# Optimization experiments

Measured on AMD Instinct MI355X. Metric: run time of the kernel, lower is better.

Reference implementation:

```python
import jax, jax.numpy as jnp
import numpy as np

N0, N1, N2 = 1200000, 120000, 12000  # nodes per hop (outermost -> seeds)
E0, E1 = 1200000, 120000
IN_C, HID_C, OUT_C = 256, 256, 64


def setup_inputs() -> dict:
    key = jax.random.key(0)
    ks = jax.random.split(key, 10)
    s_in, s_hid = 1.0 / np.sqrt(IN_C), 1.0 / np.sqrt(HID_C)
    return {
        "x": jax.random.normal(ks[0], (N0, IN_C), dtype=jnp.float32),
        "src0": jax.random.randint(ks[1], (E0,), 0, N0, dtype=jnp.int64),
        "dst0": jax.random.randint(ks[2], (E0,), 0, N1, dtype=jnp.int64),
        "src1": jax.random.randint(ks[3], (E1,), 0, N1, dtype=jnp.int64),
        "dst1": jax.random.randint(ks[4], (E1,), 0, N2, dtype=jnp.int64),
        "Wl0": jax.random.normal(ks[5], (HID_C, IN_C), dtype=jnp.float32) * s_in,
        "b0": jnp.zeros((HID_C,), dtype=jnp.float32),
        "Wr0": jax.random.normal(ks[6], (HID_C, IN_C), dtype=jnp.float32) * s_in,
        "Wl1": jax.random.normal(ks[7], (OUT_C, HID_C), dtype=jnp.float32) * s_hid,
        "b1": jnp.zeros((OUT_C,), dtype=jnp.float32),
        "Wr1": jax.random.normal(ks[8], (OUT_C, HID_C), dtype=jnp.float32) * s_hid,
    }


def _sage_conv(x_src, x_tgt, src, dst, Wl, b, Wr, n_tgt):
    # gather neighbor (source) features, mean-scatter onto targets
    msg = x_src[src]                                          # [E, C]
    agg = jax.ops.segment_sum(msg, dst, num_segments=n_tgt)   # [n_tgt, C]
    cnt = jax.ops.segment_sum(jnp.ones((dst.shape[0],), x_src.dtype), dst,
                              num_segments=n_tgt)
    agg = agg / jnp.maximum(cnt, 1.0)[:, None]
    return agg @ Wl.T + b + x_tgt @ Wr.T


def reference(x, src0, dst0, src1, dst1, Wl0, b0, Wr0, Wl1, b1, Wr1):
    # layer 0 (eval mode: dropout is identity)
    h = _sage_conv(x, x[:N1], src0, dst0, Wl0, b0, Wr0, N1)
    h = jax.nn.relu(h)
    # layer 1
    out = _sage_conv(h, h[:N2], src1, dst1, Wl1, b1, Wr1, N2)
    return jax.nn.log_softmax(out, axis=-1)
```

## Files before the change

### kernel.cpp

```cpp
#include <hip/hip_runtime.h>
#include <stdint.h>

#define N0c 1200000
#define N1c 120000
#define N2c 12000
#define E0c 1200000
#define E1c 120000
#define NB0 118
#define NB1 12
#define N1pad 120064
#define N2pad 12032
#define ROWB 80
#define ROWU 40

typedef short short8 __attribute__((ext_vector_type(8)));
typedef float f32x4 __attribute__((ext_vector_type(4)));
typedef unsigned short u16;

__device__ __forceinline__ u16 f2bf(float f) {
    union { float f; unsigned u; } v; v.f = f;
    unsigned r = v.u + 0x7FFFu + ((v.u >> 16) & 1u);
    return (u16)(r >> 16);
}
__device__ __forceinline__ float bf2f(u16 h) {
    union { unsigned u; float f; } v; v.u = ((unsigned)h) << 16;
    return v.f;
}

__device__ __forceinline__ void gload16(const char* g, char* l) {
    __builtin_amdgcn_global_load_lds(
        (const __attribute__((address_space(1))) void*)g,
        (__attribute__((address_space(3))) void*)l, 16, 0, 0);
}

__global__ void k_hist(const int* __restrict__ dst0, const int* __restrict__ dst1,
                       int* __restrict__ c0, int* __restrict__ c1) {
    int i = blockIdx.x * 256 + threadIdx.x;
    int part = blockIdx.x & 7;
    if (i < E0c) atomicAdd(&c0[part * N1c + dst0[i]], 1);
    else if (i < E0c + E1c) atomicAdd(&c1[part * N2c + dst1[i - E0c]], 1);
}

__global__ void k_scanA(const int* __restrict__ c0, const int* __restrict__ c1,
                        int* __restrict__ partials) {
    __shared__ int sh[256];
    int hop = blockIdx.x >= NB0;
    int blk = hop ? blockIdx.x - NB0 : blockIdx.x;
    const int* c = hop ? c1 : c0;
    int n = hop ? N2c : N1c;
    int d0 = blk * 1024 + threadIdx.x * 4;
    int tsum = 0;
#pragma unroll
    for (int j = 0; j < 4; ++j) {
        int d = d0 + j;
        if (d < n)
#pragma unroll
            for (int k = 0; k < 8; ++k) tsum += c[k * n + d];
    }
    sh[threadIdx.x] = tsum;
    __syncthreads();
    for (int ofs = 128; ofs > 0; ofs >>= 1) {
        if (threadIdx.x < ofs) sh[threadIdx.x] += sh[threadIdx.x + ofs];
        __syncthreads();
    }
    if (threadIdx.x == 0) partials[blockIdx.x] = sh[0];
}

__global__ void k_scanB(int* __restrict__ partials, int* __restrict__ rs0,
                        int* __restrict__ rs1) {
    __shared__ int sh[256];
    int tid = threadIdx.x;
    int v0 = tid < NB0 ? partials[tid] : 0;
    sh[tid] = v0; __syncthreads();
    for (int ofs = 1; ofs < 256; ofs <<= 1) {
        int t = tid >= ofs ? sh[tid - ofs] : 0;
        __syncthreads();
        sh[tid] += t;
        __syncthreads();
    }
    if (tid < NB0) partials[tid] = sh[tid] - v0;
    __syncthreads();
    int v1 = tid < NB1 ? partials[NB0 + tid] : 0;
    sh[tid] = v1; __syncthreads();
    for (int ofs = 1; ofs < 256; ofs <<= 1) {
        int t = tid >= ofs ? sh[tid - ofs] : 0;
        __syncthreads();
        sh[tid] += t;
        __syncthreads();
    }
    if (tid < NB1) partials[NB0 + tid] = sh[tid] - v1;
    if (tid == 0) { rs0[N1c] = E0c; rs1[N2c] = E1c; }
}

__global__ void k_scanC(const int* __restrict__ c0, const int* __restrict__ c1,
                        const int* __restrict__ partials, int* __restrict__ rs0,
                        int* __restrict__ rs1, int* __restrict__ bs0,
                        int* __restrict__ bs1) {
    __shared__ int sh[256];
    int hop = blockIdx.x >= NB0;
    int blk = hop ? blockIdx.x - NB0 : blockIdx.x;
    const int* c = hop ? c1 : c0;
    int* rs = hop ? rs1 : rs0;
    int* bs = hop ? bs1 : bs0;
    int n = hop ? N2c : N1c;
    int tid = threadIdx.x;
    int d0 = blk * 1024 + tid * 4;
    int cv[4][8];
    int tsum = 0;
#pragma unroll
    for (int j = 0; j < 4; ++j)
#pragma unroll
        for (int k = 0; k < 8; ++k) {
            int d = d0 + j;
            int v = (d < n) ? c[k * n + d] : 0;
            cv[j][k] = v; tsum += v;
        }
    sh[tid] = tsum; __syncthreads();
    for (int ofs = 1; ofs < 256; ofs <<= 1) {
        int t = tid >= ofs ? sh[tid - ofs] : 0;
        __syncthreads();
        sh[tid] += t;
        __syncthreads();
    }
    int run = partials[blockIdx.x] + sh[tid] - tsum;
#pragma unroll
    for (int j = 0; j < 4; ++j) {
        int d = d0 + j;
        if (d < n) {
            rs[d] = run;
#pragma unroll
            for (int k = 0; k < 8; ++k) { bs[k * n + d] = run; run += cv[j][k]; }
        }
    }
}

__global__ void k_scat(const int* __restrict__ src0, const int* __restrict__ dst0,
                       const int* __restrict__ src1, const int* __restrict__ dst1,
                       int* __restrict__ c0, int* __restrict__ c1,
                       const int* __restrict__ bs0, const int* __restrict__ bs1,
                       int* __restrict__ eidx0, int* __restrict__ eidx1) {
    int i = blockIdx.x * 256 + threadIdx.x;
    int part = blockIdx.x & 7;
    if (i < E0c) {
        int d = dst0[i];
        int off = atomicSub(&c0[part * N1c + d], 1) - 1;
        eidx0[bs0[part * N1c + d] + off] = src0[i];
    } else if (i < E0c + E1c) {
        int j = i - E0c;
        int d = dst1[j];
        int off = atomicSub(&c1[part * N2c + d], 1) - 1;
        eidx1[bs1[part * N2c + d] + off] = src1[j];
    }
}

__global__ void k_wcat2(u16* __restrict__ Bt0, const float* __restrict__ Wl0,
                        const float* __restrict__ Wr0, u16* __restrict__ Bt1,
                        const float* __restrict__ Wl1, const float* __restrict__ Wr1) {
    int i = blockIdx.x * blockDim.x + threadIdx.x;
    if (i < 256 * 512) {
        int c = i >> 9, k = i & 511;
        float v = (k < 256) ? Wl0[c * 256 + k] : Wr0[c * 256 + (k - 256)];
        Bt0[((size_t)(k >> 5) * 256 + c) * ROWU + (k & 31)] = f2bf(v);
    } else if (i < 256 * 512 + 128 * 512) {
        int j = i - 256 * 512;
        int c = j >> 9, k = j & 511;
        float v = 0.f;
        if (c < 64) v = (k < 256) ? Wl1[c * 256 + k] : Wr1[c * 256 + (k - 256)];
        Bt1[j] = f2bf(v);
    }
}

__global__ void k_agg0(const float* __restrict__ x, const int* __restrict__ eidx,
                       const int* __restrict__ rs, u16* __restrict__ A, int ntgt) {
    int w = (int)((blockIdx.x * blockDim.x + threadIdx.x) >> 6);
    int lane = threadIdx.x & 63;
    if (w >= ntgt) return;
    int s = rs[w], e = rs[w + 1];
    float a0 = 0.f, a1 = 0.f, a2 = 0.f, a3 = 0.f;
    int i = s;
    for (; i + 8 <= e; i += 8) {
        float4 v[8];
#pragma unroll
        for (int u = 0; u < 8; ++u)
            v[u] = ((const float4*)(x + (long)eidx[i + u] * 256))[lane];
#pragma unroll
        for (int u = 0; u < 8; ++u) {
            a0 += v[u].x; a1 += v[u].y; a2 += v[u].z; a3 += v[u].w;
        }
    }
    for (; i + 2 <= e; i += 2) {
        float4 v0 = ((const float4*)(x + (long)eidx[i] * 256))[lane];
        float4 v1 = ((const float4*)(x + (long)eidx[i + 1] * 256))[lane];
        a0 += v0.x + v1.x; a1 += v0.y + v1.y; a2 += v0.z + v1.z; a3 += v0.w + v1.w;
    }
    if (i < e) {
        float4 v = ((const float4*)(x + (long)eidx[i] * 256))[lane];
        a0 += v.x; a1 += v.y; a2 += v.z; a3 += v.w;
    }
    int c = e - s; if (c < 1) c = 1;
    float sc = 1.f / (float)c;
    int kt = lane >> 3;
    int cu = (lane & 7) * 4;
    ushort4 oa;
    oa.x = f2bf(a0 * sc); oa.y = f2bf(a1 * sc); oa.z = f2bf(a2 * sc); oa.w = f2bf(a3 * sc);
    *(ushort4*)(A + ((size_t)kt * N1pad + w) * ROWU + cu) = oa;
    float4 sv = ((const float4*)(x + (long)w * 256))[lane];
    ushort4 os;
    os.x = f2bf(sv.x); os.y = f2bf(sv.y); os.z = f2bf(sv.z); os.w = f2bf(sv.w);
    *(ushort4*)(A + ((size_t)(kt + 8) * N1pad + w) * ROWU + cu) = os;
}

__global__ void k_agg1(const u16* __restrict__ hsrc, const int* __restrict__ eidx,
                       const int* __restrict__ rs, u16* __restrict__ A, int ntgt) {
    int w = (int)((blockIdx.x * blockDim.x + threadIdx.x) >> 6);
    int lane = threadIdx.x & 63;
    if (w >= ntgt) return;
    int s = rs[w], e = rs[w + 1];
    float a0 = 0.f, a1 = 0.f, a2 = 0.f, a3 = 0.f;
    int i = s;
    for (; i + 4 <= e; i += 4) {
        ushort4 v0 = ((const ushort4*)(hsrc + (long)eidx[i] * 256))[lane];
        ushort4 v1 = ((const ushort4*)(hsrc + (long)eidx[i + 1] * 256))[lane];
        ushort4 v2 = ((const ushort4*)(hsrc + (long)eidx[i + 2] * 256))[lane];
        ushort4 v3 = ((const ushort4*)(hsrc + (long)eidx[i + 3] * 256))[lane];
        a0 += (bf2f(v0.x) + bf2f(v1.x)) + (bf2f(v2.x) + bf2f(v3.x));
        a1 += (bf2f(v0.y) + bf2f(v1.y)) + (bf2f(v2.y) + bf2f(v3.y));
        a2 += (bf2f(v0.z) + bf2f(v1.z)) + (bf2f(v2.z) + bf2f(v3.z));
        a3 += (bf2f(v0.w) + bf2f(v1.w)) + (bf2f(v2.w) + bf2f(v3.w));
    }
    for (; i < e; ++i) {
        ushort4 v = ((const ushort4*)(hsrc + (long)eidx[i] * 256))[lane];
        a0 += bf2f(v.x); a1 += bf2f(v.y); a2 += bf2f(v.z); a3 += bf2f(v.w);
    }
    int c = e - s; if (c < 1) c = 1;
    float sc = 1.f / (float)c;
    ushort4 o;
    o.x = f2bf(a0 * sc); o.y = f2bf(a1 * sc); o.z = f2bf(a2 * sc); o.w = f2bf(a3 * sc);
    *(ushort4*)(A + (long)w * 512 + lane * 4) = o;
    ushort4 sv = ((const ushort4*)(hsrc + (long)w * 256))[lane];
    *(ushort4*)(A + (long)w * 512 + 256 + lane * 4) = sv;
}

__global__ __launch_bounds__(512)
void k_gemm0(const u16* __restrict__ A0, const u16* __restrict__ Bt,
             const float* __restrict__ bias, u16* __restrict__ outp) {
    __shared__ int4 Lbuf[2 * 30720 / 16];
    char* L = (char*)Lbuf;
    const int tid = threadIdx.x;
    const int lane = tid & 63, wid = tid >> 6;
    const int wm = wid >> 2, wn = wid & 3;
    const long m0 = (long)blockIdx.x * 128;

    f32x4 acc[4][4];
#pragma unroll
    for (int i = 0; i < 4; ++i)
#pragma unroll
        for (int j = 0; j < 4; ++j) acc[i][j] = (f32x4){0.f, 0.f, 0.f, 0.f};

    const char* Abase = (const char*)A0 + m0 * ROWB;
    const char* Bbase = (const char*)Bt;

    auto stage = [&](int buf, int kt) {
        char* lb = L + buf * 30720;
        const char* ga = Abase + (size_t)kt * ((size_t)N1pad * ROWB);
        const char* gb = Bbase + (size_t)kt * (256 * ROWB);
#pragma unroll
        for (int c0 = 0; c0 < 4; ++c0) {
            int c = wid + c0 * 8;
            if (c < 30) {
                const char* g = (c < 10) ? (ga + c * 1024) : (gb + (c - 10) * 1024);
                gload16(g + lane * 16, lb + c * 1024);
            }
        }
    };

    stage(0, 0);
    const int rr = lane & 15, gg = lane >> 4;
    for (int ks = 0; ks < 16; ++ks) {
        int cur = ks & 1;
        __syncthreads();
        if (ks + 1 < 16) stage(cur ^ 1, ks + 1);
        const char* lb = L + cur * 30720;
        short8 af[4], bv[4];
#pragma unroll
        for (int f = 0; f < 4; ++f) {
            af[f] = *(const short8*)(lb + (wm * 64 + f * 16 + rr) * ROWB + gg * 16);
            bv[f] = *(const short8*)(lb + 10240 + (wn * 64 + f * 16 + rr) * ROWB + gg * 16);
        }
#pragma unroll
        for (int i = 0; i < 4; ++i)
#pragma unroll
            for (int j = 0; j < 4; ++j)
                acc[i][j] =
                    __builtin_amdgcn_mfma_f32_16x16x32_bf16(af[i], bv[j], acc[i][j], 0, 0, 0);
    }

#pragma unroll
    for (int j = 0; j < 4; ++j) {
        int col = wn * 64 + j * 16 + rr;
        float bvl = bias[col];
#pragma unroll
        for (int i = 0; i < 4; ++i) {
            long row = m0 + wm * 64 + i * 16 + gg * 4;
#pragma unroll
            for (int q = 0; q < 4; ++q) {
                long r = row + q;
                if (r < N1c) {
                    float v = acc[i][j][q] + bvl;
                    v = v > 0.f ? v : 0.f;
                    outp[r * 256 + col] = f2bf(v);
                }
            }
        }
    }
}

#define BM 128
#define BK 32
#define LDK 40

template <int WN, bool RELU_BF16>
__global__ __launch_bounds__(128 * WN)
void k_gemm(const u16* __restrict__ A, const u16* __restrict__ Bt,
            const float* __restrict__ bias, void* __restrict__ outp,
            int M, int Ncols, int ldo) {
    constexpr int BN_ = WN * 64;
    constexpr int APT = 4 / WN;
    constexpr int WSH = (WN == 4) ? 2 : 1;
    __shared__ u16 As[BM * LDK];
    __shared__ u16 Bs[BN_ * LDK];
    const int tid = threadIdx.x;
    const int lane = tid & 63, wid = tid >> 6;
    const int wm = wid >> WSH, wn = wid & (WN - 1);
    const long m0 = (long)blockIdx.x * BM;
    const int n0 = blockIdx.y * BN_;
    const int sar = tid / WN, sac = (tid % WN) * (APT * 8);
    const int sbr = tid >> 1, sbc = (tid & 1) * 16;

    f32x4 acc[4][4];
#pragma unroll
    for (int i = 0; i < 4; ++i)
#pragma unroll
        for (int j = 0; j < 4; ++j) acc[i][j] = (f32x4){0.f, 0.f, 0.f, 0.f};

    int4 ra[APT]; int4 rb[2];

    auto load_tile = [&](int ks) {
        int k0 = ks * BK;
        const int4* p = (const int4*)(A + (m0 + sar) * 512 + k0 + sac);
#pragma unroll
        for (int t = 0; t < APT; ++t) ra[t] = p[t];
        const int4* q = (const int4*)(Bt + (long)(n0 + sbr) * 512 + k0 + sbc);
        rb[0] = q[0]; rb[1] = q[1];
    };

    auto write_tile = [&]() {
        int4* da = (int4*)(As + sar * LDK + sac);
#pragma unroll
        for (int t = 0; t < APT; ++t) da[t] = ra[t];
        int4* db = (int4*)(Bs + sbr * LDK + sbc);
        db[0] = rb[0]; db[1] = rb[1];
    };

    load_tile(0);
    const int NK = 512 / BK;
    for (int ks = 0; ks < NK; ++ks) {
        __syncthreads();
        write_tile();
        __syncthreads();
        if (ks + 1 < NK) load_tile(ks + 1);
        short8 af[4], bv[4];
        const int rr = lane & 15, gg = lane >> 4;
#pragma unroll
        for (int f = 0; f < 4; ++f) {
            af[f] = *(const short8*)(As + (wm * 64 + f * 16 + rr) * LDK + gg * 8);
            bv[f] = *(const short8*)(Bs + (wn * 64 + f * 16 + rr) * LDK + gg * 8);
        }
#pragma unroll
        for (int i = 0; i < 4; ++i)
#pragma unroll
            for (int j = 0; j < 4; ++j)
                acc[i][j] =
                    __builtin_amdgcn_mfma_f32_16x16x32_bf16(af[i], bv[j], acc[i][j], 0, 0, 0);
    }

#pragma unroll
    for (int j = 0; j < 4; ++j) {
        int col = n0 + wn * 64 + j * 16 + (lane & 15);
        if (col >= Ncols) continue;
        float bvl = bias[col];
#pragma unroll
        for (int i = 0; i < 4; ++i) {
            long row = m0 + wm * 64 + i * 16 + (lane >> 4) * 4;
#pragma unroll
            for (int q = 0; q < 4; ++q) {
                long r = row + q;
                if (r < M) {
                    float v = acc[i][j][q] + bvl;
                    if (RELU_BF16) {
                        v = v > 0.f ? v : 0.f;
                        ((u16*)outp)[r * (long)ldo + col] = f2bf(v);
                    } else {
                        ((float*)outp)[r * (long)ldo + col] = v;
                    }
                }
            }
        }
    }
}

__global__ void k_lsm(const float* __restrict__ lg, float* __restrict__ out, int nrows) {
    int w = (int)((blockIdx.x * blockDim.x + threadIdx.x) >> 6);
    int lane = threadIdx.x & 63;
    if (w >= nrows) return;
    float v = lg[(long)w * 64 + lane];
    float m = v;
    for (int d = 32; d > 0; d >>= 1) m = fmaxf(m, __shfl_xor(m, d, 64));
    float ex = __expf(v - m);
    float s = ex;
    for (int d = 32; d > 0; d >>= 1) s += __shfl_xor(s, d, 64);
    out[(long)w * 64 + lane] = v - m - __logf(s);
}

extern "C" void kernel_launch(void* const* d_in, const int* in_sizes, int n_in,
                              void* d_out, int out_size, void* d_ws, size_t ws_size,
                              hipStream_t stream) {
    const float* x   = (const float*)d_in[0];
    const int* src0  = (const int*)d_in[1];
    const int* dst0  = (const int*)d_in[2];
    const int* src1  = (const int*)d_in[3];
    const int* dst1  = (const int*)d_in[4];
    const float* Wl0 = (const float*)d_in[5];
    const float* b0  = (const float*)d_in[6];
    const float* Wr0 = (const float*)d_in[7];
    const float* Wl1 = (const float*)d_in[8];
    const float* b1  = (const float*)d_in[9];
    const float* Wr1 = (const float*)d_in[10];

    char* base = (char*)d_ws;
    size_t off = 0;
    auto alloc = [&](size_t bytes) -> void* {
        off = (off + 255) & ~(size_t)255;
        void* p = base + off;
        off += bytes;
        return p;
    };
    int* c0       = (int*)alloc((size_t)8 * N1c * 4);
    int* c1       = (int*)alloc((size_t)8 * N2c * 4);
    int* bs0      = (int*)alloc((size_t)8 * N1c * 4);
    int* bs1      = (int*)alloc((size_t)8 * N2c * 4);
    int* rs0      = (int*)alloc((size_t)(N1c + 1) * 4);
    int* rs1      = (int*)alloc((size_t)(N2c + 1) * 4);
    int* partials = (int*)alloc((size_t)(NB0 + NB1) * 4);
    int* eidx0    = (int*)alloc((size_t)E0c * 4);
    int* eidx1    = (int*)alloc((size_t)E1c * 4);
    u16* A0       = (u16*)alloc((size_t)16 * N1pad * ROWU * 2);
    u16* hbuf     = (u16*)alloc((size_t)N1pad * 256 * 2);
    u16* A1       = (u16*)alloc((size_t)N2pad * 512 * 2);
    u16* Bt0      = (u16*)alloc((size_t)16 * 256 * ROWU * 2);
    u16* Bt1      = (u16*)alloc((size_t)128 * 512 * 2);
    float* logits = (float*)alloc((size_t)N2pad * 64 * 4);

    hipMemsetAsync(c0, 0, (size_t)8 * (N1c + N2c) * 4, stream);

    const int Etot = E0c + E1c;
    k_hist<<<(Etot + 255) / 256, 256, 0, stream>>>(dst0, dst1, c0, c1);
    k_scanA<<<NB0 + NB1, 256, 0, stream>>>(c0, c1, partials);
    k_scanB<<<1, 256, 0, stream>>>(partials, rs0, rs1);
    k_scanC<<<NB0 + NB1, 256, 0, stream>>>(c0, c1, partials, rs0, rs1, bs0, bs1);
    k_scat<<<(Etot + 255) / 256, 256, 0, stream>>>(src0, dst0, src1, dst1,
                                                   c0, c1, bs0, bs1, eidx0, eidx1);

    k_wcat2<<<(256 * 512 + 128 * 512 + 255) / 256, 256, 0, stream>>>(Bt0, Wl0, Wr0,
                                                                     Bt1, Wl1, Wr1);

    k_agg0<<<(N1c + 3) / 4, 256, 0, stream>>>(x, eidx0, rs0, A0, N1c);
    k_gemm0<<<N1pad / 128, 512, 0, stream>>>(A0, Bt0, b0, hbuf);

    k_agg1<<<(N2c + 3) / 4, 256, 0, stream>>>(hbuf, eidx1, rs1, A1, N2c);
    dim3 g1(N2pad / BM, 1);
    k_gemm<2, false><<<g1, 256, 0, stream>>>(A1, Bt1, b1, logits, N2c, 64, 64);

    k_lsm<<<(N2c + 3) / 4, 256, 0, stream>>>(logits, (float*)d_out, N2c);
}
```

Measured before the change: 584.7 us.

## Fuse weight prep into histogram, self-features into GEMM0, log-softmax into GEMM1

Merges the weight conversion kernel into the histogram launch as extra blocks. The layer-0 self-feature bf16 conversion moves from the aggregation kernel into the GEMM0 staging path, which now reads x directly for the upper K tiles. This halves the A0 buffer and removes a write and re-read. It also specializes the second GEMM with a fused bias and log-softmax epilogue, dropping the logits buffer and the separate softmax kernel. Gather loads in agg0 switch to nontemporal loads, which risks worse cache behaviour for repeated source rows, and GEMM0 staging now does synchronous register loads for half its K tiles.

```diff
diff --git a/kernel.cpp b/kernel.cpp
--- a/kernel.cpp
+++ b/kernel.cpp
@@ -12,6 +12,8 @@
 #define N2pad 12032
 #define ROWB 80
 #define ROWU 40
+#define HB 5157
+#define WCB 768
 
 typedef short short8 __attribute__((ext_vector_type(8)));
 typedef float f32x4 __attribute__((ext_vector_type(4)));
@@ -22,10 +24,6 @@
     unsigned r = v.u + 0x7FFFu + ((v.u >> 16) & 1u);
     return (u16)(r >> 16);
 }
-__device__ __forceinline__ float bf2f(u16 h) {
-    union { unsigned u; float f; } v; v.u = ((unsigned)h) << 16;
-    return v.f;
-}
 
 __device__ __forceinline__ void gload16(const char* g, char* l) {
     __builtin_amdgcn_global_load_lds(
@@ -34,11 +32,29 @@
 }
 
 __global__ void k_hist(const int* __restrict__ dst0, const int* __restrict__ dst1,
-                       int* __restrict__ c0, int* __restrict__ c1) {
-    int i = blockIdx.x * 256 + threadIdx.x;
-    int part = blockIdx.x & 7;
-    if (i < E0c) atomicAdd(&c0[part * N1c + dst0[i]], 1);
-    else if (i < E0c + E1c) atomicAdd(&c1[part * N2c + dst1[i - E0c]], 1);
+                       int* __restrict__ c0, int* __restrict__ c1,
+                       u16* __restrict__ Bt0, const float* __restrict__ Wl0,
+                       const float* __restrict__ Wr0, u16* __restrict__ Bt1,
+                       const float* __restrict__ Wl1, const float* __restrict__ Wr1) {
+    if (blockIdx.x < HB) {
+        int i = blockIdx.x * 256 + threadIdx.x;
+        int part = blockIdx.x & 7;
+        if (i < E0c) atomicAdd(&c0[part * N1c + dst0[i]], 1);
+        else if (i < E0c + E1c) atomicAdd(&c1[part * N2c + dst1[i - E0c]], 1);
+    } else {
+        int i = (blockIdx.x - HB) * 256 + threadIdx.x;
+        if (i < 256 * 512) {
+            int c = i >> 9, k = i & 511;
+            float v = (k < 256) ? Wl0[c * 256 + k] : Wr0[c * 256 + (k - 256)];
+            Bt0[((size_t)(k >> 5) * 256 + c) * ROWU + (k & 31)] = f2bf(v);
+        } else {
+            int j = i - 256 * 512;
+            int c = j >> 9, k = j & 511;
+            float v = 0.f;
+            if (c < 64) v = (k < 256) ? Wl1[c * 256 + k] : Wr1[c * 256 + (k - 256)];
+            Bt1[j] = f2bf(v);
+        }
+    }
 }
 
 __global__ void k_scanA(const int* __restrict__ c0, const int* __restrict__ c1,
@@ -153,23 +169,6 @@
     }
 }
 
-__global__ void k_wcat2(u16* __restrict__ Bt0, const float* __restrict__ Wl0,
-                        const float* __restrict__ Wr0, u16* __restrict__ Bt1,
-                        const float* __restrict__ Wl1, const float* __restrict__ Wr1) {
-    int i = blockIdx.x * blockDim.x + threadIdx.x;
-    if (i < 256 * 512) {
-        int c = i >> 9, k = i & 511;
-        float v = (k < 256) ? Wl0[c * 256 + k] : Wr0[c * 256 + (k - 256)];
-        Bt0[((size_t)(k >> 5) * 256 + c) * ROWU + (k & 31)] = f2bf(v);
-    } else if (i < 256 * 512 + 128 * 512) {
-        int j = i - 256 * 512;
-        int c = j >> 9, k = j & 511;
-        float v = 0.f;
-        if (c < 64) v = (k < 256) ? Wl1[c * 256 + k] : Wr1[c * 256 + (k - 256)];
-        Bt1[j] = f2bf(v);
-    }
-}
-
 __global__ void k_agg0(const float* __restrict__ x, const int* __restrict__ eidx,
                        const int* __restrict__ rs, u16* __restrict__ A, int ntgt) {
     int w = (int)((blockIdx.x * blockDim.x + threadIdx.x) >> 6);
@@ -179,23 +178,28 @@
     float a0 = 0.f, a1 = 0.f, a2 = 0.f, a3 = 0.f;
     int i = s;
     for (; i + 8 <= e; i += 8) {
-        float4 v[8];
+        f32x4 v[8];
 #pragma unroll
         for (int u = 0; u < 8; ++u)
-            v[u] = ((const float4*)(x + (long)eidx[i + u] * 256))[lane];
+            v[u] = __builtin_nontemporal_load(
+                ((const f32x4*)(x + (long)eidx[i + u] * 256)) + lane);
 #pragma unroll
         for (int u = 0; u < 8; ++u) {
-            a0 += v[u].x; a1 += v[u].y; a2 += v[u].z; a3 += v[u].w;
+            a0 += v[u][0]; a1 += v[u][1]; a2 += v[u][2]; a3 += v[u][3];
         }
     }
     for (; i + 2 <= e; i += 2) {
-        float4 v0 = ((const float4*)(x + (long)eidx[i] * 256))[lane];
-        float4 v1 = ((const float4*)(x + (long)eidx[i + 1] * 256))[lane];
-        a0 += v0.x + v1.x; a1 += v0.y + v1.y; a2 += v0.z + v1.z; a3 += v0.w + v1.w;
+        f32x4 v0 = __builtin_nontemporal_load(
+            ((const f32x4*)(x + (long)eidx[i] * 256)) + lane);
+        f32x4 v1 = __builtin_nontemporal_load(
+            ((const f32x4*)(x + (long)eidx[i + 1] * 256)) + lane);
+        a0 += v0[0] + v1[0]; a1 += v0[1] + v1[1];
+        a2 += v0[2] + v1[2]; a3 += v0[3] + v1[3];
     }
     if (i < e) {
-        float4 v = ((const float4*)(x + (long)eidx[i] * 256))[lane];
-        a0 += v.x; a1 += v.y; a2 += v.z; a3 += v.w;
+        f32x4 v = __builtin_nontemporal_load(
+            ((const f32x4*)(x + (long)eidx[i] * 256)) + lane);
+        a0 += v[0]; a1 += v[1]; a2 += v[2]; a3 += v[3];
     }
     int c = e - s; if (c < 1) c = 1;
     float sc = 1.f / (float)c;
@@ -204,10 +208,6 @@
     ushort4 oa;
     oa.x = f2bf(a0 * sc); oa.y = f2bf(a1 * sc); oa.z = f2bf(a2 * sc); oa.w = f2bf(a3 * sc);
     *(ushort4*)(A + ((size_t)kt * N1pad + w) * ROWU + cu) = oa;
-    float4 sv = ((const float4*)(x + (long)w * 256))[lane];
-    ushort4 os;
-    os.x = f2bf(sv.x); os.y = f2bf(sv.y); os.z = f2bf(sv.z); os.w = f2bf(sv.w);
-    *(ushort4*)(A + ((size_t)(kt + 8) * N1pad + w) * ROWU + cu) = os;
 }
 
 __global__ void k_agg1(const u16* __restrict__ hsrc, const int* __restrict__ eidx,
@@ -217,20 +217,23 @@
     if (w >= ntgt) return;
     int s = rs[w], e = rs[w + 1];
     float a0 = 0.f, a1 = 0.f, a2 = 0.f, a3 = 0.f;
+    auto acc4 = [&](ushort4 v) {
+        union { unsigned u; float f; } c0, c1, c2, c3;
+        c0.u = (unsigned)v.x << 16; c1.u = (unsigned)v.y << 16;
+        c2.u = (unsigned)v.z << 16; c3.u = (unsigned)v.w << 16;
+        a0 += c0.f; a1 += c1.f; a2 += c2.f; a3 += c3.f;
+    };
     int i = s;
     for (; i + 4 <= e; i += 4) {
         ushort4 v0 = ((const ushort4*)(hsrc + (long)eidx[i] * 256))[lane];
         ushort4 v1 = ((const ushort4*)(hsrc + (long)eidx[i + 1] * 256))[lane];
         ushort4 v2 = ((const ushort4*)(hsrc + (long)eidx[i + 2] * 256))[lane];
         ushort4 v3 = ((const ushort4*)(hsrc + (long)eidx[i + 3] * 256))[lane];
-        a0 += (bf2f(v0.x) + bf2f(v1.x)) + (bf2f(v2.x) + bf2f(v3.x));
-        a1 += (bf2f(v0.y) + bf2f(v1.y)) + (bf2f(v2.y) + bf2f(v3.y));
-        a2 += (bf2f(v0.z) + bf2f(v1.z)) + (bf2f(v2.z) + bf2f(v3.z));
-        a3 += (bf2f(v0.w) + bf2f(v1.w)) + (bf2f(v2.w) + bf2f(v3.w));
+        acc4(v0); acc4(v1); acc4(v2); acc4(v3);
     }
     for (; i < e; ++i) {
         ushort4 v = ((const ushort4*)(hsrc + (long)eidx[i] * 256))[lane];
-        a0 += bf2f(v.x); a1 += bf2f(v.y); a2 += bf2f(v.z); a3 += bf2f(v.w);
+        acc4(v);
     }
     int c = e - s; if (c < 1) c = 1;
     float sc = 1.f / (float)c;
@@ -242,8 +245,9 @@
 }
 
 __global__ __launch_bounds__(512)
-void k_gemm0(const u16* __restrict__ A0, const u16* __restrict__ Bt,
-             const float* __restrict__ bias, u16* __restrict__ outp) {
+void k_gemm0(const u16* __restrict__ A0, const float* __restrict__ x,
+             const u16* __restrict__ Bt, const float* __restrict__ bias,
+             u16* __restrict__ outp) {
     __shared__ int4 Lbuf[2 * 30720 / 16];
     char* L = (char*)Lbuf;
     const int tid = threadIdx.x;
@@ -259,18 +263,35 @@
 
     const char* Abase = (const char*)A0 + m0 * ROWB;
     const char* Bbase = (const char*)Bt;
+    const int srow = tid >> 2, scq = tid & 3;
 
     auto stage = [&](int buf, int kt) {
         char* lb = L + buf * 30720;
-        const char* ga = Abase + (size_t)kt * ((size_t)N1pad * ROWB);
         const char* gb = Bbase + (size_t)kt * (256 * ROWB);
-#pragma unroll
-        for (int c0 = 0; c0 < 4; ++c0) {
-            int c = wid + c0 * 8;
-            if (c < 30) {
-                const char* g = (c < 10) ? (ga + c * 1024) : (gb + (c - 10) * 1024);
-                gload16(g + lane * 16, lb + c * 1024);
+        if (kt < 8) {
+            const char* ga = Abase + (size_t)kt * ((size_t)N1pad * ROWB);
+#pragma unroll
+            for (int c0 = 0; c0 < 4; ++c0) {
+                int c = wid + c0 * 8;
+                if (c < 30) {
+                    const char* g = (c < 10) ? (ga + c * 1024) : (gb + (c - 10) * 1024);
+                    gload16(g + lane * 16, lb + c * 1024);
+                }
             }
+        } else {
+#pragma unroll
+            for (int c0 = 0; c0 < 3; ++c0) {
+                int c = wid + c0 * 8;
+                if (c < 20) gload16(gb + c * 1024 + lane * 16, lb + 10240 + c * 1024);
+            }
+            const f32x4* p =
+                (const f32x4*)(x + (m0 + srow) * 256 + (kt - 8) * 32 + scq * 8);
+            f32x4 v0 = p[0], v1 = p[1];
+            ushort4 h0, h1;
+            h0.x = f2bf(v0[0]); h0.y = f2bf(v0[1]); h0.z = f2bf(v0[2]); h0.w = f2bf(v0[3]);
+            h1.x = f2bf(v1[0]); h1.y = f2bf(v1[1]); h1.z = f2bf(v1[2]); h1.w = f2bf(v1[3]);
+            ushort4* d = (ushort4*)(lb + srow * ROWB + scq * 16);
+            d[0] = h0; d[1] = h1;
         }
     };
 
@@ -315,27 +336,16 @@
     }
 }
 
-#define BM 128
-#define BK 32
-#define LDK 40
-
-template <int WN, bool RELU_BF16>
-__global__ __launch_bounds__(128 * WN)
-void k_gemm(const u16* __restrict__ A, const u16* __restrict__ Bt,
-            const float* __restrict__ bias, void* __restrict__ outp,
-            int M, int Ncols, int ldo) {
-    constexpr int BN_ = WN * 64;
-    constexpr int APT = 4 / WN;
-    constexpr int WSH = (WN == 4) ? 2 : 1;
-    __shared__ u16 As[BM * LDK];
-    __shared__ u16 Bs[BN_ * LDK];
+__global__ __launch_bounds__(256)
+void k_gemm1(const u16* __restrict__ A, const u16* __restrict__ Bt,
+             const float* __restrict__ bias, float* __restrict__ outp) {
+    __shared__ u16 As[128 * 40];
+    __shared__ u16 Bs[128 * 40];
     const int tid = threadIdx.x;
     const int lane = tid & 63, wid = tid >> 6;
-    const int wm = wid >> WSH, wn = wid & (WN - 1);
-    const long m0 = (long)blockIdx.x * BM;
-    const int n0 = blockIdx.y * BN_;
-    const int sar = tid / WN, sac = (tid % WN) * (APT * 8);
-    const int sbr = tid >> 1, sbc = (tid & 1) * 16;
+    const int wm = wid >> 1, wn = wid & 1;
+    const long m0 = (long)blockIdx.x * 128;
+    const int sar = tid >> 1, sac = (tid & 1) * 16;
 
     f32x4 acc[4][4];
 #pragma unroll
@@ -343,38 +353,33 @@
 #pragma unroll
         for (int j = 0; j < 4; ++j) acc[i][j] = (f32x4){0.f, 0.f, 0.f, 0.f};
 
-    int4 ra[APT]; int4 rb[2];
-
+    int4 ra[2]; int4 rb[2];
     auto load_tile = [&](int ks) {
-        int k0 = ks * BK;
+        int k0 = ks * 32;
         const int4* p = (const int4*)(A + (m0 + sar) * 512 + k0 + sac);
-#pragma unroll
-        for (int t = 0; t < APT; ++t) ra[t] = p[t];
-        const int4* q = (const int4*)(Bt + (long)(n0 + sbr) * 512 + k0 + sbc);
+        ra[0] = p[0]; ra[1] = p[1];
+        const int4* q = (const int4*)(Bt + (long)sar * 512 + k0 + sac);
         rb[0] = q[0]; rb[1] = q[1];
     };
-
     auto write_tile = [&]() {
-        int4* da = (int4*)(As + sar * LDK + sac);
-#pragma unroll
-        for (int t = 0; t < APT; ++t) da[t] = ra[t];
-        int4* db = (int4*)(Bs + sbr * LDK + sbc);
+        int4* da = (int4*)(As + sar * 40 + sac);
+        da[0] = ra[0]; da[1] = ra[1];
+        int4* db = (int4*)(Bs + sar * 40 + sac);
         db[0] = rb[0]; db[1] = rb[1];
     };
 
     load_tile(0);
-    const int NK = 512 / BK;
-    for (int ks = 0; ks < NK; ++ks) {
+    for (int ks = 0; ks < 16; ++ks) {
         __syncthreads();
         write_tile();
         __syncthreads();
-        if (ks + 1 < NK) load_tile(ks + 1);
+        if (ks + 1 < 16) load_tile(ks + 1);
         short8 af[4], bv[4];
         const int rr = lane & 15, gg = lane >> 4;
 #pragma unroll
         for (int f = 0; f < 4; ++f) {
-            af[f] = *(const short8*)(As + (wm * 64 + f * 16 + rr) * LDK + gg * 8);
-            bv[f] = *(const short8*)(Bs + (wn * 64 + f * 16 + rr) * LDK + gg * 8);
+            af[f] = *(const short8*)(As + (wm * 64 + f * 16 + rr) * 40 + gg * 8);
+            bv[f] = *(const short8*)(Bs + (wn * 64 + f * 16 + rr) * 40 + gg * 8);
         }
 #pragma unroll
         for (int i = 0; i < 4; ++i)
@@ -384,42 +389,32 @@
                     __builtin_amdgcn_mfma_f32_16x16x32_bf16(af[i], bv[j], acc[i][j], 0, 0, 0);
     }
 
-#pragma unroll
-    for (int j = 0; j < 4; ++j) {
-        int col = n0 + wn * 64 + j * 16 + (lane & 15);
-        if (col >= Ncols) continue;
-        float bvl = bias[col];
+    const int rr = lane & 15, gg = lane >> 4;
+    if (wn == 0) {
 #pragma unroll
         for (int i = 0; i < 4; ++i) {
-            long row = m0 + wm * 64 + i * 16 + (lane >> 4) * 4;
 #pragma unroll
             for (int q = 0; q < 4; ++q) {
-                long r = row + q;
-                if (r < M) {
-                    float v = acc[i][j][q] + bvl;
-                    if (RELU_BF16) {
-                        v = v > 0.f ? v : 0.f;
-                        ((u16*)outp)[r * (long)ldo + col] = f2bf(v);
-                    } else {
-                        ((float*)outp)[r * (long)ldo + col] = v;
-                    }
+                long r = m0 + wm * 64 + i * 16 + gg * 4 + q;
+                float v[4];
+#pragma unroll
+                for (int j = 0; j < 4; ++j) v[j] = acc[i][j][q] + bias[j * 16 + rr];
+                float mx = fmaxf(fmaxf(v[0], v[1]), fmaxf(v[2], v[3]));
+#pragma unroll
+                for (int m = 1; m < 16; m <<= 1) mx = fmaxf(mx, __shfl_xor(mx, m, 16));
+                float se = __expf(v[0] - mx) + __expf(v[1] - mx) +
+                           __expf(v[2] - mx) + __expf(v[3] - mx);
+#pragma unroll
+                for (int m = 1; m < 16; m <<= 1) se += __shfl_xor(se, m, 16);
+                float ln = __logf(se);
+                if (r < N2c) {
+#pragma unroll
+                    for (int j = 0; j < 4; ++j)
+                        outp[r * 64 + j * 16 + rr] = v[j] - mx - ln;
                 }
             }
         }
     }
-}
-
-__global__ void k_lsm(const float* __restrict__ lg, float* __restrict__ out, int nrows) {
-    int w = (int)((blockIdx.x * blockDim.x + threadIdx.x) >> 6);
-    int lane = threadIdx.x & 63;
-    if (w >= nrows) return;
-    float v = lg[(long)w * 64 + lane];
-    float m = v;
-    for (int d = 32; d > 0; d >>= 1) m = fmaxf(m, __shfl_xor(m, d, 64));
-    float ex = __expf(v - m);
-    float s = ex;
-    for (int d = 32; d > 0; d >>= 1) s += __shfl_xor(s, d, 64);
-    out[(long)w * 64 + lane] = v - m - __logf(s);
 }
 
 extern "C" void kernel_launch(void* const* d_in, const int* in_sizes, int n_in,
@@ -454,32 +449,25 @@
     int* partials = (int*)alloc((size_t)(NB0 + NB1) * 4);
     int* eidx0    = (int*)alloc((size_t)E0c * 4);
     int* eidx1    = (int*)alloc((size_t)E1c * 4);
-    u16* A0       = (u16*)alloc((size_t)16 * N1pad * ROWU * 2);
+    u16* A0       = (u16*)alloc((size_t)8 * N1pad * ROWU * 2);
     u16* hbuf     = (u16*)alloc((size_t)N1pad * 256 * 2);
     u16* A1       = (u16*)alloc((size_t)N2pad * 512 * 2);
     u16* Bt0      = (u16*)alloc((size_t)16 * 256 * ROWU * 2);
     u16* Bt1      = (u16*)alloc((size_t)128 * 512 * 2);
-    float* logits = (float*)alloc((size_t)N2pad * 64 * 4);
-
-    hipMemsetAsync(c0, 0, (size_t)8 * (N1c + N2c) * 4, stream);
-
-    const int Etot = E0c + E1c;
-    k_hist<<<(Etot + 255) / 256, 256, 0, stream>>>(dst0, dst1, c0, c1);
+
+    (void)hipMemsetAsync(c0, 0, (size_t)8 * (N1c + N2c) * 4, stream);
+
+    k_hist<<<HB + WCB, 256, 0, stream>>>(dst0, dst1, c0, c1,
+                                         Bt0, Wl0, Wr0, Bt1, Wl1, Wr1);
     k_scanA<<<NB0 + NB1, 256, 0, stream>>>(c0, c1, partials);
     k_scanB<<<1, 256, 0, stream>>>(partials, rs0, rs1);
     k_scanC<<<NB0 + NB1, 256, 0, stream>>>(c0, c1, partials, rs0, rs1, bs0, bs1);
-    k_scat<<<(Etot + 255) / 256, 256, 0, stream>>>(src0, dst0, src1, dst1,
-                                                   c0, c1, bs0, bs1, eidx0, eidx1);
-
-    k_wcat2<<<(256 * 512 + 128 * 512 + 255) / 256, 256, 0, stream>>>(Bt0, Wl0, Wr0,
-                                                                     Bt1, Wl1, Wr1);
+    k_scat<<<HB, 256, 0, stream>>>(src0, dst0, src1, dst1,
+                                   c0, c1, bs0, bs1, eidx0, eidx1);
 
     k_agg0<<<(N1c + 3) / 4, 256, 0, stream>>>(x, eidx0, rs0, A0, N1c);
-    k_gemm0<<<N1pad / 128, 512, 0, stream>>>(A0, Bt0, b0, hbuf);
+    k_gemm0<<<N1pad / 128, 512, 0, stream>>>(A0, x, Bt0, b0, hbuf);
 
     k_agg1<<<(N2c + 3) / 4, 256, 0, stream>>>(hbuf, eidx1, rs1, A1, N2c);
-    dim3 g1(N2pad / BM, 1);
-    k_gemm<2, false><<<g1, 256, 0, stream>>>(A1, Bt1, b1, logits, N2c, 64, 64);
-
-    k_lsm<<<(N2c + 3) / 4, 256, 0, stream>>>(logits, (float*)d_out, N2c);
-}
+    k_gemm1<<<N2pad / 128, 256, 0, stream>>>(A1, Bt1, b1, (float*)d_out);
+}
```

Measured after the change: 533.0 us. 8.8% less time.
